# Kernel tuning notes

Hardware: AMD Instinct MI355X
Metric: run time of the kernel (lower is better)

The kernel has to match this reference:

```python
import jax, jax.numpy as jnp
import numpy as np

BZ, NF, D = 8, 10000, 16
H = W = 512


def setup_inputs() -> dict:
    key = jax.random.key(0)
    k1, k2, k3 = jax.random.split(key, 3)
    attrs = jax.random.normal(k1, (BZ, NF, 3, D), dtype=jnp.float32)
    # barycentric weights: positive, sum to 1 over the 3 vertices
    u = jax.random.uniform(k2, (BZ, H, W, 3), dtype=jnp.float32, minval=1e-3, maxval=1.0)
    baryw_buffer = u / jnp.sum(u, axis=-1, keepdims=True)
    # triangle indices into the flattened [BZ*NF] face table; -1 = empty pixel
    triangle_buffer = jax.random.randint(k3, (BZ, H, W), -1, BZ * NF, dtype=jnp.int32)
    return {"attrs": attrs, "baryw_buffer": baryw_buffer, "triangle_buffer": triangle_buffer}


def reference(attrs, baryw_buffer, triangle_buffer):
    # attrs: [N, NF, 3, D]; baryw_buffer: [N, H, W, 3]; triangle_buffer: [N, H, W] int (-1 = bg)
    N, H_, W_ = triangle_buffer.shape
    Dd = attrs.shape[-1]
    flat_attrs = attrs.reshape(-1, 3, Dd)                      # [N*NF, 3, D]
    mask = triangle_buffer == -1                               # [N, H, W]
    idx = jnp.where(mask, 0, triangle_buffer)                  # clamp bg to 0
    pixel_face_vals = flat_attrs[idx]                          # [N, H, W, 3, D] gather
    pixel_vals = jnp.einsum('nhwk,nhwkd->nhwd', baryw_buffer, pixel_face_vals)
    pixel_vals = jnp.where(mask[..., None], 0.0, pixel_vals)   # zero background
    out = jnp.moveaxis(pixel_vals, -1, 1)                      # [N, D, H, W]
    vis = (~mask).astype(jnp.float32)[:, None]                 # [N, 1, H, W]
    return jnp.concatenate([out, vis], axis=1)                 # [N, D+1, H, W]
```

## Files before the change

kernel.cpp:

```cpp
#include <hip/hip_runtime.h>
#include <hip/hip_fp16.h>

constexpr int BZ = 8, NF = 10000, D = 16, HImg = 512, WImg = 512;
constexpr int HW = HImg * WImg;
constexpr int NPIX = BZ * HW;
constexpr int NFACES = BZ * NF;
constexpr int PIX_PER_THREAD = 4;
constexpr int NTHREADS = NPIX / PIX_PER_THREAD;
constexpr int BLOCK = 256;
constexpr size_t REC_USHORTS = 64;
constexpr size_t WS_NEEDED = (size_t)NFACES * 128;

constexpr int NPHASE = 4;
constexpr int FACES_PER_PHASE = NFACES / NPHASE;

typedef float f32x4 __attribute__((ext_vector_type(4)));
typedef int   i32x4 __attribute__((ext_vector_type(4)));

__global__ __launch_bounds__(BLOCK) void convert_kernel(
    const float* __restrict__ attrs, ushort* __restrict__ rec)
{
    const int tid = blockIdx.x * BLOCK + threadIdx.x;
    if (tid >= NFACES * 6) return;
    const int face = tid / 6;
    const int c    = tid - face * 6;
    const float4* src = reinterpret_cast<const float4*>(
        attrs + (size_t)face * 48 + c * 8);
    const float4 a = src[0], b = src[1];
    __half h[8];
    h[0] = __float2half_rn(a.x); h[1] = __float2half_rn(a.y);
    h[2] = __float2half_rn(a.z); h[3] = __float2half_rn(a.w);
    h[4] = __float2half_rn(b.x); h[5] = __float2half_rn(b.y);
    h[6] = __float2half_rn(b.z); h[7] = __float2half_rn(b.w);
    *reinterpret_cast<int4*>(rec + (size_t)face * REC_USHORTS + c * 8) =
        *reinterpret_cast<const int4*>(h);
}

__device__ inline void h8_to_f8(int4 raw, float f[8]) {
    const __half2* hp = reinterpret_cast<const __half2*>(&raw);
#pragma unroll
    for (int q = 0; q < 4; ++q) {
        const float2 t = __half22float2(hp[q]);
        f[2 * q]     = t.x;
        f[2 * q + 1] = t.y;
    }
}

__global__ __launch_bounds__(BLOCK) void render_f16_phased_kernel(
    const ushort* __restrict__ rec,
    const float*  __restrict__ baryw,
    const int*    __restrict__ tri,
    float*        __restrict__ out)
{
    const int tid = blockIdx.x * BLOCK + threadIdx.x;
    const int p0  = tid * PIX_PER_THREAD;

    const int n   = p0 / HW;
    const int pix = p0 - n * HW;

    const i32x4 t4 = __builtin_nontemporal_load(
        reinterpret_cast<const i32x4*>(tri + p0));
    const f32x4* bw = reinterpret_cast<const f32x4*>(baryw + (size_t)p0 * 3);
    const f32x4 b0 = __builtin_nontemporal_load(bw + 0);
    const f32x4 b1 = __builtin_nontemporal_load(bw + 1);
    const f32x4 b2 = __builtin_nontemporal_load(bw + 2);

    float w[PIX_PER_THREAD][3] = {
        {b0.x, b0.y, b0.z},
        {b0.w, b1.x, b1.y},
        {b1.z, b1.w, b2.x},
        {b2.y, b2.z, b2.w},
    };
    const int t[PIX_PER_THREAD] = {t4.x, t4.y, t4.z, t4.w};

    float vis[PIX_PER_THREAD];
#pragma unroll
    for (int j = 0; j < PIX_PER_THREAD; ++j) {
        const bool bg = (t[j] < 0);
        vis[j] = bg ? 0.0f : 1.0f;
        w[j][0] *= vis[j];
        w[j][1] *= vis[j];
        w[j][2] *= vis[j];
    }

    const size_t outbase = (size_t)n * (D + 1) * HW + pix;
    const int4* rec4 = reinterpret_cast<const int4*>(rec);

#pragma unroll
    for (int c = 0; c < 2; ++c) {
        float r[PIX_PER_THREAD][8];
#pragma unroll
        for (int j = 0; j < PIX_PER_THREAD; ++j)
#pragma unroll
            for (int i = 0; i < 8; ++i) r[j][i] = 0.0f;

#pragma unroll
        for (int ph = 0; ph < NPHASE; ++ph) {
            const int lo = ph * FACES_PER_PHASE;
#pragma unroll
            for (int j = 0; j < PIX_PER_THREAD; ++j) {
                if ((unsigned)(t[j] - lo) < (unsigned)FACES_PER_PHASE) {
                    const int4* rb = rec4 + (size_t)t[j] * 8;
                    const int4 A0 = rb[0 + c];
                    const int4 A1 = rb[2 + c];
                    const int4 A2 = rb[4 + c];
                    float a0[8], a1[8], a2[8];
                    h8_to_f8(A0, a0);
                    h8_to_f8(A1, a1);
                    h8_to_f8(A2, a2);
#pragma unroll
                    for (int i = 0; i < 8; ++i)
                        r[j][i] += w[j][0] * a0[i] + w[j][1] * a1[i]
                                 + w[j][2] * a2[i];
                }
            }
            if (ph != NPHASE - 1) __syncthreads();
        }

#pragma unroll
        for (int i = 0; i < 8; ++i) {
            const int d = c * 8 + i;
            f32x4 o;
            o.x = r[0][i]; o.y = r[1][i]; o.z = r[2][i]; o.w = r[3][i];
            __builtin_nontemporal_store(
                o, reinterpret_cast<f32x4*>(out + outbase + (size_t)d * HW));
        }
        if (c == 0) __syncthreads();
    }

    f32x4 v;
    v.x = vis[0]; v.y = vis[1]; v.z = vis[2]; v.w = vis[3];
    __builtin_nontemporal_store(
        v, reinterpret_cast<f32x4*>(out + outbase + (size_t)D * HW));
}

__global__ __launch_bounds__(BLOCK) void renderer_f32_kernel(
    const float* __restrict__ attrs,
    const float* __restrict__ baryw,
    const int*   __restrict__ tri,
    float*       __restrict__ out)
{
    const int tid = blockIdx.x * BLOCK + threadIdx.x;
    const int p0  = tid * PIX_PER_THREAD;
    if (p0 >= NPIX) return;

    const int n   = p0 / HW;
    const int pix = p0 - n * HW;

    const int4 t4 = *reinterpret_cast<const int4*>(tri + p0);
    const float4* bw = reinterpret_cast<const float4*>(baryw + (size_t)p0 * 3);
    const float4 b0 = bw[0], b1 = bw[1], b2 = bw[2];

    float w[PIX_PER_THREAD][3] = {
        {b0.x, b0.y, b0.z},
        {b0.w, b1.x, b1.y},
        {b1.z, b1.w, b2.x},
        {b2.y, b2.z, b2.w},
    };
    const int t[PIX_PER_THREAD] = {t4.x, t4.y, t4.z, t4.w};

    float vis[PIX_PER_THREAD];
    const float4* abase[PIX_PER_THREAD];
#pragma unroll
    for (int j = 0; j < PIX_PER_THREAD; ++j) {
        const bool bg = (t[j] < 0);
        vis[j] = bg ? 0.0f : 1.0f;
        const int tc = bg ? 0 : t[j];
        abase[j] = reinterpret_cast<const float4*>(attrs + (size_t)tc * (3 * D));
        w[j][0] *= vis[j];
        w[j][1] *= vis[j];
        w[j][2] *= vis[j];
    }

    const size_t outbase = (size_t)n * (D + 1) * HW + pix;

#pragma unroll
    for (int c = 0; c < 4; ++c) {
        float r[PIX_PER_THREAD][4];
#pragma unroll
        for (int j = 0; j < PIX_PER_THREAD; ++j) {
            const float4 a0 = abase[j][c];
            const float4 a1 = abase[j][4 + c];
            const float4 a2 = abase[j][8 + c];
            r[j][0] = w[j][0] * a0.x + w[j][1] * a1.x + w[j][2] * a2.x;
            r[j][1] = w[j][0] * a0.y + w[j][1] * a1.y + w[j][2] * a2.y;
            r[j][2] = w[j][0] * a0.z + w[j][1] * a1.z + w[j][2] * a2.z;
            r[j][3] = w[j][0] * a0.w + w[j][1] * a1.w + w[j][2] * a2.w;
        }
#pragma unroll
        for (int i = 0; i < 4; ++i) {
            const int d = c * 4 + i;
            float4 o;
            o.x = r[0][i]; o.y = r[1][i]; o.z = r[2][i]; o.w = r[3][i];
            *reinterpret_cast<float4*>(out + outbase + (size_t)d * HW) = o;
        }
    }

    float4 v;
    v.x = vis[0]; v.y = vis[1]; v.z = vis[2]; v.w = vis[3];
    *reinterpret_cast<float4*>(out + outbase + (size_t)D * HW) = v;
}

extern "C" void kernel_launch(void* const* d_in, const int* in_sizes, int n_in,
                              void* d_out, int out_size, void* d_ws, size_t ws_size,
                              hipStream_t stream) {
    const float* attrs = (const float*)d_in[0];
    const float* baryw = (const float*)d_in[1];
    const int*   tri   = (const int*)d_in[2];
    float*       out   = (float*)d_out;

    const int grid = NTHREADS / BLOCK;

    if (ws_size >= WS_NEEDED) {
        ushort* rec = (ushort*)d_ws;
        const int conv_grid = (NFACES * 6 + BLOCK - 1) / BLOCK;
        convert_kernel<<<conv_grid, BLOCK, 0, stream>>>(attrs, rec);
        render_f16_phased_kernel<<<grid, BLOCK, 0, stream>>>(rec, baryw, tri, out);
    } else {
        renderer_f32_kernel<<<grid, BLOCK, 0, stream>>>(attrs, baryw, tri, out);
    }
}
```

Before: 217.5 us.

## Gather all sixteen channels in a single phased sweep over faces

Merges the two channel-half passes into one sweep, so each face record (96 bytes of fp16) is fetched in full once per pixel instead of in two halves across two phased sweeps. This halves the number of phase loops and barriers and removes the second traversal of the face table. The cost is 64 accumulators plus six int4 loads per pixel group held in registers. A launch-bounds occupancy hint of 4 is added to keep register pressure in check, which risks spills.

```diff
diff --git a/kernel.cpp b/kernel.cpp
--- a/kernel.cpp
+++ b/kernel.cpp
@@ -46,7 +46,7 @@
     }
 }
 
-__global__ __launch_bounds__(BLOCK) void render_f16_phased_kernel(
+__global__ __launch_bounds__(BLOCK, 4) void render_f16_sweep_kernel(
     const ushort* __restrict__ rec,
     const float*  __restrict__ baryw,
     const int*    __restrict__ tri,
@@ -83,51 +83,51 @@
         w[j][2] *= vis[j];
     }
 
-    const size_t outbase = (size_t)n * (D + 1) * HW + pix;
     const int4* rec4 = reinterpret_cast<const int4*>(rec);
 
-#pragma unroll
-    for (int c = 0; c < 2; ++c) {
-        float r[PIX_PER_THREAD][8];
-#pragma unroll
-        for (int j = 0; j < PIX_PER_THREAD; ++j)
-#pragma unroll
-            for (int i = 0; i < 8; ++i) r[j][i] = 0.0f;
-
-#pragma unroll
-        for (int ph = 0; ph < NPHASE; ++ph) {
-            const int lo = ph * FACES_PER_PHASE;
-#pragma unroll
-            for (int j = 0; j < PIX_PER_THREAD; ++j) {
-                if ((unsigned)(t[j] - lo) < (unsigned)FACES_PER_PHASE) {
-                    const int4* rb = rec4 + (size_t)t[j] * 8;
-                    const int4 A0 = rb[0 + c];
-                    const int4 A1 = rb[2 + c];
-                    const int4 A2 = rb[4 + c];
-                    float a0[8], a1[8], a2[8];
-                    h8_to_f8(A0, a0);
-                    h8_to_f8(A1, a1);
-                    h8_to_f8(A2, a2);
-#pragma unroll
-                    for (int i = 0; i < 8; ++i)
-                        r[j][i] += w[j][0] * a0[i] + w[j][1] * a1[i]
-                                 + w[j][2] * a2[i];
+    float r[PIX_PER_THREAD][D];
+#pragma unroll
+    for (int j = 0; j < PIX_PER_THREAD; ++j)
+#pragma unroll
+        for (int i = 0; i < D; ++i) r[j][i] = 0.0f;
+
+#pragma unroll
+    for (int ph = 0; ph < NPHASE; ++ph) {
+        const int lo = ph * FACES_PER_PHASE;
+#pragma unroll
+        for (int j = 0; j < PIX_PER_THREAD; ++j) {
+            if ((unsigned)(t[j] - lo) < (unsigned)FACES_PER_PHASE) {
+                const int4* rb = rec4 + (size_t)t[j] * 8;
+                const int4 V0 = rb[0];
+                const int4 V1 = rb[1];
+                const int4 V2 = rb[2];
+                const int4 V3 = rb[3];
+                const int4 V4 = rb[4];
+                const int4 V5 = rb[5];
+                float a0[8], a1[8], a2[8], a3[8], a4[8], a5[8];
+                h8_to_f8(V0, a0); h8_to_f8(V1, a1);
+                h8_to_f8(V2, a2); h8_to_f8(V3, a3);
+                h8_to_f8(V4, a4); h8_to_f8(V5, a5);
+#pragma unroll
+                for (int i = 0; i < 8; ++i) {
+                    r[j][i]     += w[j][0] * a0[i] + w[j][1] * a2[i]
+                                 + w[j][2] * a4[i];
+                    r[j][8 + i] += w[j][0] * a1[i] + w[j][1] * a3[i]
+                                 + w[j][2] * a5[i];
                 }
             }
-            if (ph != NPHASE - 1) __syncthreads();
         }
-
-#pragma unroll
-        for (int i = 0; i < 8; ++i) {
-            const int d = c * 8 + i;
-            f32x4 o;
-            o.x = r[0][i]; o.y = r[1][i]; o.z = r[2][i]; o.w = r[3][i];
-            __builtin_nontemporal_store(
-                o, reinterpret_cast<f32x4*>(out + outbase + (size_t)d * HW));
-        }
-        if (c == 0) __syncthreads();
-    }
-
+        if (ph != NPHASE - 1) __syncthreads();
+    }
+
+    const size_t outbase = (size_t)n * (D + 1) * HW + pix;
+#pragma unroll
+    for (int d = 0; d < D; ++d) {
+        f32x4 o;
+        o.x = r[0][d]; o.y = r[1][d]; o.z = r[2][d]; o.w = r[3][d];
+        __builtin_nontemporal_store(
+            o, reinterpret_cast<f32x4*>(out + outbase + (size_t)d * HW));
+    }
     f32x4 v;
     v.x = vis[0]; v.y = vis[1]; v.z = vis[2]; v.w = vis[3];
     __builtin_nontemporal_store(
@@ -215,7 +215,7 @@
         ushort* rec = (ushort*)d_ws;
         const int conv_grid = (NFACES * 6 + BLOCK - 1) / BLOCK;
         convert_kernel<<<conv_grid, BLOCK, 0, stream>>>(attrs, rec);
-        render_f16_phased_kernel<<<grid, BLOCK, 0, stream>>>(rec, baryw, tri, out);
+        render_f16_sweep_kernel<<<grid, BLOCK, 0, stream>>>(rec, baryw, tri, out);
     } else {
         renderer_f32_kernel<<<grid, BLOCK, 0, stream>>>(attrs, baryw, tri, out);
     }
```

Result: faster. 208.6 us (median of 2 runs) (-4.1%).

## Split feature channels across wave halves to double thread parallelism

Applied to the files above, without the earlier changes.

Each pixel quad is now handled by two lanes, one per 8-channel half of the feature dimension, instead of one thread looping over both halves. This doubles the thread count, removes the per-thread channel loop and one barrier, and adds an occupancy hint to launch bounds, aiming to expose more memory-level parallelism for the gathers. The cost is that tri and baryw are loaded twice (once per half-wave), which adds input traffic.

```diff
diff --git a/kernel.cpp b/kernel.cpp
--- a/kernel.cpp
+++ b/kernel.cpp
@@ -5,9 +5,9 @@
 constexpr int HW = HImg * WImg;
 constexpr int NPIX = BZ * HW;
 constexpr int NFACES = BZ * NF;
-constexpr int PIX_PER_THREAD = 4;
-constexpr int NTHREADS = NPIX / PIX_PER_THREAD;
+constexpr int PIX_PER_LANE = 4;
 constexpr int BLOCK = 256;
+constexpr int NTHREADS = NPIX * 2 / PIX_PER_LANE;
 constexpr size_t REC_USHORTS = 64;
 constexpr size_t WS_NEEDED = (size_t)NFACES * 128;
 
@@ -46,14 +46,19 @@
     }
 }
 
-__global__ __launch_bounds__(BLOCK) void render_f16_phased_kernel(
+__global__ __launch_bounds__(BLOCK, 4) void render_split_kernel(
     const ushort* __restrict__ rec,
     const float*  __restrict__ baryw,
     const int*    __restrict__ tri,
     float*        __restrict__ out)
 {
-    const int tid = blockIdx.x * BLOCK + threadIdx.x;
-    const int p0  = tid * PIX_PER_THREAD;
+    const int tidx = threadIdx.x;
+    const int lane = tidx & 63;
+    const int wid  = tidx >> 6;
+    const int h    = lane >> 5;
+    const int q    = lane & 31;
+    const int wave = blockIdx.x * (BLOCK / 64) + wid;
+    const int p0   = wave * (64 * PIX_PER_LANE / 2) + q * PIX_PER_LANE;
 
     const int n   = p0 / HW;
     const int pix = p0 - n * HW;
@@ -65,17 +70,17 @@
     const f32x4 b1 = __builtin_nontemporal_load(bw + 1);
     const f32x4 b2 = __builtin_nontemporal_load(bw + 2);
 
-    float w[PIX_PER_THREAD][3] = {
+    float w[PIX_PER_LANE][3] = {
         {b0.x, b0.y, b0.z},
         {b0.w, b1.x, b1.y},
         {b1.z, b1.w, b2.x},
         {b2.y, b2.z, b2.w},
     };
-    const int t[PIX_PER_THREAD] = {t4.x, t4.y, t4.z, t4.w};
-
-    float vis[PIX_PER_THREAD];
-#pragma unroll
-    for (int j = 0; j < PIX_PER_THREAD; ++j) {
+    const int t[PIX_PER_LANE] = {t4.x, t4.y, t4.z, t4.w};
+
+    float vis[PIX_PER_LANE];
+#pragma unroll
+    for (int j = 0; j < PIX_PER_LANE; ++j) {
         const bool bg = (t[j] < 0);
         vis[j] = bg ? 0.0f : 1.0f;
         w[j][0] *= vis[j];
@@ -83,55 +88,52 @@
         w[j][2] *= vis[j];
     }
 
+    const int4* rec4 = reinterpret_cast<const int4*>(rec);
+
+    float r[PIX_PER_LANE][8];
+#pragma unroll
+    for (int j = 0; j < PIX_PER_LANE; ++j)
+#pragma unroll
+        for (int i = 0; i < 8; ++i) r[j][i] = 0.0f;
+
+#pragma unroll
+    for (int ph = 0; ph < NPHASE; ++ph) {
+        const int lo = ph * FACES_PER_PHASE;
+#pragma unroll
+        for (int j = 0; j < PIX_PER_LANE; ++j) {
+            if ((unsigned)(t[j] - lo) < (unsigned)FACES_PER_PHASE) {
+                const int4* rb = rec4 + (size_t)t[j] * 8 + h;
+                const int4 V0 = rb[0];
+                const int4 V1 = rb[2];
+                const int4 V2 = rb[4];
+                float a0[8], a1[8], a2[8];
+                h8_to_f8(V0, a0);
+                h8_to_f8(V1, a1);
+                h8_to_f8(V2, a2);
+#pragma unroll
+                for (int i = 0; i < 8; ++i)
+                    r[j][i] += w[j][0] * a0[i] + w[j][1] * a1[i]
+                             + w[j][2] * a2[i];
+            }
+        }
+        if (ph != NPHASE - 1) __syncthreads();
+    }
+
     const size_t outbase = (size_t)n * (D + 1) * HW + pix;
-    const int4* rec4 = reinterpret_cast<const int4*>(rec);
-
-#pragma unroll
-    for (int c = 0; c < 2; ++c) {
-        float r[PIX_PER_THREAD][8];
-#pragma unroll
-        for (int j = 0; j < PIX_PER_THREAD; ++j)
-#pragma unroll
-            for (int i = 0; i < 8; ++i) r[j][i] = 0.0f;
-
-#pragma unroll
-        for (int ph = 0; ph < NPHASE; ++ph) {
-            const int lo = ph * FACES_PER_PHASE;
-#pragma unroll
-            for (int j = 0; j < PIX_PER_THREAD; ++j) {
-                if ((unsigned)(t[j] - lo) < (unsigned)FACES_PER_PHASE) {
-                    const int4* rb = rec4 + (size_t)t[j] * 8;
-                    const int4 A0 = rb[0 + c];
-                    const int4 A1 = rb[2 + c];
-                    const int4 A2 = rb[4 + c];
-                    float a0[8], a1[8], a2[8];
-                    h8_to_f8(A0, a0);
-                    h8_to_f8(A1, a1);
-                    h8_to_f8(A2, a2);
-#pragma unroll
-                    for (int i = 0; i < 8; ++i)
-                        r[j][i] += w[j][0] * a0[i] + w[j][1] * a1[i]
-                                 + w[j][2] * a2[i];
-                }
-            }
-            if (ph != NPHASE - 1) __syncthreads();
-        }
-
-#pragma unroll
-        for (int i = 0; i < 8; ++i) {
-            const int d = c * 8 + i;
-            f32x4 o;
-            o.x = r[0][i]; o.y = r[1][i]; o.z = r[2][i]; o.w = r[3][i];
-            __builtin_nontemporal_store(
-                o, reinterpret_cast<f32x4*>(out + outbase + (size_t)d * HW));
-        }
-        if (c == 0) __syncthreads();
-    }
-
-    f32x4 v;
-    v.x = vis[0]; v.y = vis[1]; v.z = vis[2]; v.w = vis[3];
-    __builtin_nontemporal_store(
-        v, reinterpret_cast<f32x4*>(out + outbase + (size_t)D * HW));
+#pragma unroll
+    for (int i = 0; i < 8; ++i) {
+        const int d = h * 8 + i;
+        f32x4 o;
+        o.x = r[0][i]; o.y = r[1][i]; o.z = r[2][i]; o.w = r[3][i];
+        __builtin_nontemporal_store(
+            o, reinterpret_cast<f32x4*>(out + outbase + (size_t)d * HW));
+    }
+    if (h == 0) {
+        f32x4 v;
+        v.x = vis[0]; v.y = vis[1]; v.z = vis[2]; v.w = vis[3];
+        __builtin_nontemporal_store(
+            v, reinterpret_cast<f32x4*>(out + outbase + (size_t)D * HW));
+    }
 }
 
 __global__ __launch_bounds__(BLOCK) void renderer_f32_kernel(
@@ -141,7 +143,7 @@
     float*       __restrict__ out)
 {
     const int tid = blockIdx.x * BLOCK + threadIdx.x;
-    const int p0  = tid * PIX_PER_THREAD;
+    const int p0  = tid * 4;
     if (p0 >= NPIX) return;
 
     const int n   = p0 / HW;
@@ -151,18 +153,18 @@
     const float4* bw = reinterpret_cast<const float4*>(baryw + (size_t)p0 * 3);
     const float4 b0 = bw[0], b1 = bw[1], b2 = bw[2];
 
-    float w[PIX_PER_THREAD][3] = {
+    float w[4][3] = {
         {b0.x, b0.y, b0.z},
         {b0.w, b1.x, b1.y},
         {b1.z, b1.w, b2.x},
         {b2.y, b2.z, b2.w},
     };
-    const int t[PIX_PER_THREAD] = {t4.x, t4.y, t4.z, t4.w};
-
-    float vis[PIX_PER_THREAD];
-    const float4* abase[PIX_PER_THREAD];
-#pragma unroll
-    for (int j = 0; j < PIX_PER_THREAD; ++j) {
+    const int t[4] = {t4.x, t4.y, t4.z, t4.w};
+
+    float vis[4];
+    const float4* abase[4];
+#pragma unroll
+    for (int j = 0; j < 4; ++j) {
         const bool bg = (t[j] < 0);
         vis[j] = bg ? 0.0f : 1.0f;
         const int tc = bg ? 0 : t[j];
@@ -176,9 +178,9 @@
 
 #pragma unroll
     for (int c = 0; c < 4; ++c) {
-        float r[PIX_PER_THREAD][4];
-#pragma unroll
-        for (int j = 0; j < PIX_PER_THREAD; ++j) {
+        float r[4][4];
+#pragma unroll
+        for (int j = 0; j < 4; ++j) {
             const float4 a0 = abase[j][c];
             const float4 a1 = abase[j][4 + c];
             const float4 a2 = abase[j][8 + c];
@@ -209,14 +211,14 @@
     const int*   tri   = (const int*)d_in[2];
     float*       out   = (float*)d_out;
 
-    const int grid = NTHREADS / BLOCK;
-
     if (ws_size >= WS_NEEDED) {
         ushort* rec = (ushort*)d_ws;
         const int conv_grid = (NFACES * 6 + BLOCK - 1) / BLOCK;
         convert_kernel<<<conv_grid, BLOCK, 0, stream>>>(attrs, rec);
-        render_f16_phased_kernel<<<grid, BLOCK, 0, stream>>>(rec, baryw, tri, out);
+        const int grid = NTHREADS / BLOCK;
+        render_split_kernel<<<grid, BLOCK, 0, stream>>>(rec, baryw, tri, out);
     } else {
+        const int grid = (NPIX / 4) / BLOCK;
         renderer_f32_kernel<<<grid, BLOCK, 0, stream>>>(attrs, baryw, tri, out);
     }
 }
```

After: 212.3 us. -2.4%, faster.
